# Performance work log

Hardware: AMD Instinct MI355X
Metric: run time of the kernel (lower is better)

## Reference

```python
import jax, jax.numpy as jnp
import numpy as np
from jax import lax


def _conv3x3(x, w, groups=1):
    # x: [B,C,H,W], w: [O, C//groups, 3, 3], padding=1, no bias
    return lax.conv_general_dilated(
        x, w, window_strides=(1, 1), padding=((1, 1), (1, 1)),
        dimension_numbers=('NCHW', 'OIHW', 'NCHW'),
        feature_group_count=groups)


def _nonlocal_attention(x):
    # q = k = v = flattened features; attn is [B, N, N] with N = H*W
    B, C, H, W = x.shape
    f = x.reshape(B, C, H * W)                                   # [B,C,N]
    attn = jax.nn.softmax(jnp.einsum('bcn,bcm->bnm', f, f), -1)  # [B,N,N]
    out = jnp.einsum('bnm,bcm->bcn', attn, f)                    # [B,C,N]
    return out.reshape(B, C, H, W)


def setup_inputs() -> dict:
    key = jax.random.key(0)
    k1, k2 = jax.random.split(key)
    C = 64
    x = jax.random.normal(k1, (8, C, 64, 64), dtype=jnp.float32)
    # kaiming_normal fan_out for 3x3 conv: std = sqrt(2 / (C*9))
    W_std = jax.random.normal(k2, (C, C, 3, 3), dtype=jnp.float32) * np.float32(np.sqrt(2.0 / (C * 9)))
    return {'x': x, 'W_std': W_std}


def reference(x, W_std):
    B, C, H, W = x.shape
    # FusionDiffConv: standard 3x3 conv + fixed depthwise Laplacian conv
    lap = jnp.array([[0., 1., 0.], [1., -4., 1.], [0., 1., 0.]], dtype=x.dtype)
    W_lap = jnp.broadcast_to(lap[None, None], (C, 1, 3, 3))
    feat = _conv3x3(x, W_std) + _conv3x3(x, W_lap, groups=C)
    # AttentionModule: 3-scale pooled non-local attention pyramid, bilinear upsample, sum
    out = jnp.zeros_like(feat)
    for scale in (4, 2, 1):
        h, w = H // scale, W // scale
        blk = feat.reshape(B, C, h, scale, w, scale).mean(axis=(3, 5))  # adaptive_avg_pool2d (exact divisor)
        blk = _nonlocal_attention(blk)
        # bilinear, half-pixel centers == torch align_corners=False
        out = out + jax.image.resize(blk, (B, C, H, W), method='bilinear')
    return x + out
```

## Files before the change

kernel.cpp:

```cpp
#include <hip/hip_runtime.h>
#include <hip/hip_bf16.h>
#include <math.h>

#define BB 8
#define CC 64
#define HH 64
#define WW 64
#define NPIX (HH*WW)
#define LOG2E 1.44269504088896340736f

typedef __attribute__((ext_vector_type(8))) short bf16x8;
typedef __attribute__((ext_vector_type(8))) _Float16 half8;
typedef __attribute__((ext_vector_type(4))) float floatx4;
typedef __attribute__((ext_vector_type(8))) unsigned short ushort8;

__device__ inline unsigned short f2bf(float x) {
  __hip_bfloat16 h = __float2bfloat16(x);
  return *reinterpret_cast<unsigned short*>(&h);
}
__device__ inline unsigned short f2bf_fast(float x) {
  const unsigned u = __float_as_uint(x);
  return (unsigned short)((u + 0x8000u) >> 16);
}
__device__ inline float bf2f(unsigned short u) {
  __hip_bfloat16 h = *reinterpret_cast<__hip_bfloat16*>(&u);
  return __bfloat162float(h);
}
__device__ inline unsigned short f2h(float x) {
  _Float16 h = (_Float16)x;
  return *reinterpret_cast<unsigned short*>(&h);
}
__device__ inline float h2f(unsigned short u) {
  _Float16 h = *reinterpret_cast<_Float16*>(&u);
  return (float)h;
}

__device__ inline int swzoff(int n, int c) {
  return (((c >> 3) ^ (n & 7)) << 3) | (c & 7);
}
__device__ inline int swzvslot(int key, int c) {
  return (((key >> 3) ^ (c & 7)) << 3) | (key & 7);
}

#define GLD_LDS16(gp, lp)                                                     \
  __builtin_amdgcn_global_load_lds(                                           \
      (const __attribute__((address_space(1))) void*)(gp),                    \
      (__attribute__((address_space(3))) void*)(lp), 16, 0, 0)

__global__ __launch_bounds__(256) void prep_kernel(
    const float* __restrict__ xin, const float* __restrict__ w,
    unsigned short* __restrict__ xth, unsigned short* __restrict__ xtl,
    unsigned short* __restrict__ wth, unsigned short* __restrict__ wtl) {
  __shared__ float XL[64][65];
  const int bid = blockIdx.x;
  const int tid = threadIdx.x;
  if (bid < 512) {
    const int y = bid & 63, b = bid >> 6;
    const int xq = tid & 15, cw = tid >> 4;
    const float* xb = xin + (size_t)b * CC * NPIX + y * WW;
#pragma unroll
    for (int p = 0; p < 4; ++p) {
      const int c = p * 16 + cw;
      const float4 v = *(const float4*)(xb + (size_t)c * NPIX + xq * 4);
      XL[c][xq * 4 + 0] = v.x; XL[c][xq * 4 + 1] = v.y;
      XL[c][xq * 4 + 2] = v.z; XL[c][xq * 4 + 3] = v.w;
    }
    __syncthreads();
    const int px = tid & 63, cp = tid >> 6;
    const size_t nb = ((size_t)b * NPIX + y * WW + px) * CC;
    ushort8 vh[2], vl[2];
#pragma unroll
    for (int j = 0; j < 16; ++j) {
      const float v = XL[cp * 16 + j][px];
      const unsigned short hh = f2bf(v);
      vh[j >> 3][j & 7] = hh;
      vl[j >> 3][j & 7] = f2bf(v - bf2f(hh));
    }
#pragma unroll
    for (int k = 0; k < 2; ++k) {
      const int ch = cp * 2 + k;
      const int off = ((ch ^ (px & 7)) << 3);
      *(ushort8*)(xth + nb + off) = vh[k];
      *(ushort8*)(xtl + nb + off) = vl[k];
    }
  } else {
    const int idx = (bid - 512) * 256 + tid;
    const int c   = idx & 63;
    const int o   = (idx >> 6) & 63;
    const int tap = idx >> 12;
    float v = w[((o * 64 + c) * 9) + tap];
    if (o == c) {
      const float lapk[9] = {0.f, 1.f, 0.f, 1.f, -4.f, 1.f, 0.f, 1.f, 0.f};
      v += lapk[tap];
    }
    const unsigned short hi = f2bf(v);
    wth[(tap * 64 + o) * 64 + c] = hi;
    wtl[(tap * 64 + o) * 64 + c] = f2bf(v - bf2f(hi));
  }
}

__global__ __launch_bounds__(256, 2) void conv_mfma(
    const unsigned short* __restrict__ xth,
    const unsigned short* __restrict__ xtl,
    const unsigned short* __restrict__ wth,
    const unsigned short* __restrict__ wtl,
    unsigned short* __restrict__ fh, unsigned short* __restrict__ fl,
    unsigned short* __restrict__ fv) {
  __shared__ __align__(16) unsigned short XS[6 * 4096];

  const int tid  = threadIdx.x;
  const int lane = tid & 63;
  const int wave = tid >> 6;
  const int r16  = lane & 15;
  const int quad = lane >> 4;
  const int y = blockIdx.x, b = blockIdx.y;

#pragma unroll
  for (int r = 0; r < 3; ++r) {
    const int yy = min(max(y - 1 + r, 0), HH - 1);
    const unsigned short* sh = xth + ((size_t)b * NPIX + yy * WW) * CC;
    const unsigned short* sl = xtl + ((size_t)b * NPIX + yy * WW) * CC;
    GLD_LDS16(sh + tid * 8,        &XS[r * 4096 + tid * 8]);
    GLD_LDS16(sh + 2048 + tid * 8, &XS[r * 4096 + 2048 + tid * 8]);
    GLD_LDS16(sl + tid * 8,        &XS[(3 + r) * 4096 + tid * 8]);
    GLD_LDS16(sl + 2048 + tid * 8, &XS[(3 + r) * 4096 + 2048 + tid * 8]);
  }
  __syncthreads();

  floatx4 acc[4];
#pragma unroll
  for (int t = 0; t < 4; ++t) acc[t] = (floatx4){0.f, 0.f, 0.f, 0.f};
  const bf16x8 ZF = {0, 0, 0, 0, 0, 0, 0, 0};
  const int og = wave * 16 + r16;

#pragma unroll
  for (int tap = 0; tap < 9; ++tap) {
    const int ky = tap / 3, kx = tap % 3;
    const int yy = y + ky - 1;
    if (yy < 0 || yy >= HH) continue;
    const unsigned short* wt = wth + ((tap * 64 + og) << 6);
    const unsigned short* wl = wtl + ((tap * 64 + og) << 6);
    const bf16x8 Wh0 = *(const bf16x8*)(wt + quad * 8);
    const bf16x8 Wh1 = *(const bf16x8*)(wt + 32 + quad * 8);
    const bf16x8 Wl0 = *(const bf16x8*)(wl + quad * 8);
    const bf16x8 Wl1 = *(const bf16x8*)(wl + 32 + quad * 8);
#pragma unroll
    for (int t = 0; t < 4; ++t) {
      const int px = t * 16 + r16 + kx - 1;
      const bool ok = (px >= 0) && (px < WW);
      const int pxc = ok ? px : 0;
      const int bh = ky * 4096 + pxc * 64;
      const int bl = bh + 3 * 4096;
      const int o0 = ((quad ^ (pxc & 7)) << 3);
      const int o1 = (((4 + quad) ^ (pxc & 7)) << 3);
      bf16x8 Ah0 = *(const bf16x8*)(XS + bh + o0);
      bf16x8 Ah1 = *(const bf16x8*)(XS + bh + o1);
      bf16x8 Al0 = *(const bf16x8*)(XS + bl + o0);
      bf16x8 Al1 = *(const bf16x8*)(XS + bl + o1);
      if (!ok) { Ah0 = ZF; Ah1 = ZF; Al0 = ZF; Al1 = ZF; }
      acc[t] = __builtin_amdgcn_mfma_f32_16x16x32_bf16(Ah0, Wh0, acc[t], 0, 0, 0);
      acc[t] = __builtin_amdgcn_mfma_f32_16x16x32_bf16(Ah1, Wh1, acc[t], 0, 0, 0);
      acc[t] = __builtin_amdgcn_mfma_f32_16x16x32_bf16(Ah0, Wl0, acc[t], 0, 0, 0);
      acc[t] = __builtin_amdgcn_mfma_f32_16x16x32_bf16(Ah1, Wl1, acc[t], 0, 0, 0);
      acc[t] = __builtin_amdgcn_mfma_f32_16x16x32_bf16(Al0, Wh0, acc[t], 0, 0, 0);
      acc[t] = __builtin_amdgcn_mfma_f32_16x16x32_bf16(Al1, Wh1, acc[t], 0, 0, 0);
    }
  }

#pragma unroll
  for (int t = 0; t < 4; ++t)
#pragma unroll
    for (int r = 0; r < 4; ++r) {
      const int key = t * 16 + quad * 4 + r;
      const int n = y * WW + key;
      const float v = acc[t][r];
      const unsigned short hi = f2h(v);
      const unsigned short lo = f2h(v - h2f(hi));
      fh[((size_t)b * NPIX + n) * CC + swzoff(n, og)] = hi;
      fl[((size_t)b * NPIX + n) * CC + swzoff(n, og)] = lo;
      fv[(((size_t)b * (NPIX >> 6) + y) * CC + og) * 64 + swzvslot(key, og)] =
          f2bf(v);
    }
}

__global__ void pools_kernel(const unsigned short* __restrict__ in_h,
                             const unsigned short* __restrict__ in_l,
                             unsigned short* __restrict__ h2,
                             unsigned short* __restrict__ l2,
                             unsigned short* __restrict__ v2,
                             unsigned short* __restrict__ h4,
                             unsigned short* __restrict__ l4,
                             unsigned short* __restrict__ v4) {
  const int bid = blockIdx.x;
  if (bid < 2048) {
    const int idx = bid * 256 + threadIdx.x;
    const int c  = idx & 63;
    const int t  = idx >> 6;
    const int xo = t & 31;
    const int yo = (t >> 5) & 31;
    const int b  = t >> 10;
    const size_t ibase = (size_t)b * NPIX * CC;
    float s = 0.f;
#pragma unroll
    for (int dy = 0; dy < 2; ++dy)
#pragma unroll
      for (int dx = 0; dx < 2; ++dx) {
        const int nin = (2*yo+dy) * 64 + (2*xo+dx);
        const size_t a = ibase + (size_t)nin * CC + swzoff(nin, c);
        s += h2f(in_h[a]) + h2f(in_l[a]);
      }
    const float vv = 0.25f * s;
    const unsigned short hi = f2h(vv);
    const int nout = yo * 32 + xo;
    const size_t ob = ((size_t)b * 1024 + nout) * CC + swzoff(nout, c);
    h2[ob] = hi;
    l2[ob] = f2h(vv - h2f(hi));
    v2[(((size_t)b * 16 + (nout >> 6)) * CC + c) * 64 + swzvslot(nout & 63, c)] =
        f2bf(vv);
  } else {
    const int idx = (bid - 2048) * 256 + threadIdx.x;
    const int c  = idx & 63;
    const int t  = idx >> 6;
    const int xo = t & 15;
    const int yo = (t >> 4) & 15;
    const int b  = t >> 8;
    const size_t ibase = (size_t)b * NPIX * CC;
    float s = 0.f;
#pragma unroll
    for (int dy = 0; dy < 4; ++dy)
#pragma unroll
      for (int dx = 0; dx < 4; ++dx) {
        const int nin = (4*yo+dy) * 64 + (4*xo+dx);
        const size_t a = ibase + (size_t)nin * CC + swzoff(nin, c);
        s += h2f(in_h[a]) + h2f(in_l[a]);
      }
    const float vv = 0.0625f * s;
    const unsigned short hi = f2h(vv);
    const int nout = yo * 16 + xo;
    const size_t ob = ((size_t)b * 256 + nout) * CC + swzoff(nout, c);
    h4[ob] = hi;
    l4[ob] = f2h(vv - h2f(hi));
    v4[(((size_t)b * 4 + (nout >> 6)) * CC + c) * 64 + swzvslot(nout & 63, c)] =
        f2bf(vv);
  }
}

#define STR 72

template <int NH, int KS>
__device__ __forceinline__ void attn_body(
    int bid,
    const unsigned short* __restrict__ fh,
    const unsigned short* __restrict__ fl,
    const unsigned short* __restrict__ fv,
    float* __restrict__ outF, unsigned short* __restrict__ outB,
    float* __restrict__ outL, int N,
    unsigned short* KVT, unsigned short* PtB) {
  const int tid  = threadIdx.x;
  const int lane = tid & 63;
  const int wave = tid >> 6;
  const int b    = bid & 7;
  const int rest = bid >> 3;
  const int nq   = N / (64 * NH);
  const int qt   = rest % nq;
  const int ks   = rest / nq;
  const int q0   = qt * (64 * NH) + wave * (16 * NH);
  const int nt   = (N >> 6) / KS;
  const int t0   = ks * nt;
  const int r16  = lane & 15;
  const int quad = lane >> 4;
  const int swb  = r16 & 7;

  const unsigned short* fhB = fh + (size_t)b * N * CC;
  const unsigned short* flB = fl + (size_t)b * N * CC;
  const unsigned short* fvB = fv + (size_t)b * N * CC;

  {
    const size_t tb = (size_t)t0 * 4096;
#pragma unroll
    for (int j = 0; j < 4; ++j) {
      const int cid = wave * 4 + j;
      const int arr = cid >> 3, sub = (cid & 7) << 9;
      const unsigned short* g = (arr == 0 ? fhB : fvB) + tb + sub + lane * 8;
      GLD_LDS16(g, KVT + arr * 4096 + sub + lane * 8);
    }
  }

  half8 Qh[NH][2], Ql[NH][2];
  float Mq[NH][4];
#pragma unroll
  for (int h = 0; h < NH; ++h) {
    float Mpart = 0.f;
#pragma unroll
    for (int kss = 0; kss < 2; ++kss) {
      const size_t off = (size_t)(q0 + h * 16 + r16) * CC
                         + ((((kss << 2) + quad) ^ swb) << 3);
      const ushort8 hh = *(const ushort8*)(fhB + off);
      const ushort8 ll = *(const ushort8*)(flB + off);
      half8 sh, sl;
#pragma unroll
      for (int j = 0; j < 8; ++j) {
        const float f = h2f(hh[j]) + h2f(ll[j]);
        const float g = f * LOG2E;
        const _Float16 gh = (_Float16)g;
        sh[j] = gh;
        sl[j] = (_Float16)(g - (float)gh);
        Mpart += g * f;
      }
      Qh[h][kss] = sh;
      Ql[h][kss] = sl;
    }
    Mpart += __shfl_xor(Mpart, 16, 64);
    Mpart += __shfl_xor(Mpart, 32, 64);
#pragma unroll
    for (int r = 0; r < 4; ++r) Mq[h][r] = __shfl(Mpart, quad * 4 + r, 64);
  }

  floatx4 O[NH][4];
  float lrun[NH][4];
#pragma unroll
  for (int h = 0; h < NH; ++h)
#pragma unroll
    for (int ch = 0; ch < 4; ++ch) {
      O[h][ch] = (floatx4){0.f, 0.f, 0.f, 0.f};
      lrun[h][ch] = 0.f;
    }
  unsigned short* ptw = PtB + wave * (NH * 16 * STR);

  int koff[2];
#pragma unroll
  for (int kss = 0; kss < 2; ++kss) koff[kss] = (((kss << 2) + quad) ^ swb) << 3;

  for (int t = 0; t < nt; ++t) {
    const int cur = t & 1;
    __syncthreads();
    if (t + 1 < nt) {
      const size_t tb = (size_t)(t0 + t + 1) * 4096;
      unsigned short* dst = KVT + (cur ^ 1) * 8192;
#pragma unroll
      for (int j = 0; j < 4; ++j) {
        const int cid = wave * 4 + j;
        const int arr = cid >> 3, sub = (cid & 7) << 9;
        const unsigned short* g = (arr == 0 ? fhB : fvB) + tb + sub + lane * 8;
        GLD_LDS16(g, dst + arr * 4096 + sub + lane * 8);
      }
    }
    const unsigned short* kh = KVT + cur * 8192;
    const unsigned short* vt = kh + 4096;

#pragma unroll
    for (int tt = 0; tt < 4; ++tt) {
      const int kbase = (tt * 16 + r16) * 64;
      const half8 Kh0 = *(const half8*)(kh + kbase + koff[0]);
      const half8 Kh1 = *(const half8*)(kh + kbase + koff[1]);
#pragma unroll
      for (int h = 0; h < NH; ++h) {
        floatx4 s = (floatx4){0.f, 0.f, 0.f, 0.f};
        s = __builtin_amdgcn_mfma_f32_16x16x32_f16(Qh[h][0], Kh0, s, 0, 0, 0);
        s = __builtin_amdgcn_mfma_f32_16x16x32_f16(Qh[h][1], Kh1, s, 0, 0, 0);
        s = __builtin_amdgcn_mfma_f32_16x16x32_f16(Ql[h][0], Kh0, s, 0, 0, 0);
        s = __builtin_amdgcn_mfma_f32_16x16x32_f16(Ql[h][1], Kh1, s, 0, 0, 0);
        unsigned short* pth = ptw + h * (16 * STR);
#pragma unroll
        for (int r = 0; r < 4; ++r) {
          const float p = __builtin_amdgcn_exp2f(s[r] - Mq[h][r]);
          lrun[h][r] += p;
          pth[(quad * 4 + r) * STR + tt * 16 + r16] = f2bf_fast(p);
        }
      }
    }

    bf16x8 Pf[NH][2];
#pragma unroll
    for (int h = 0; h < NH; ++h)
#pragma unroll
      for (int kss = 0; kss < 2; ++kss)
        Pf[h][kss] = *(const bf16x8*)(ptw + h * (16 * STR) + r16 * STR
                                      + kss * 32 + quad * 8);
#pragma unroll
    for (int kss = 0; kss < 2; ++kss)
#pragma unroll
      for (int ch = 0; ch < 4; ++ch) {
        const bf16x8 Vf = *(const bf16x8*)(vt + (ch * 16 + r16) * 64 + koff[kss]);
#pragma unroll
        for (int h = 0; h < NH; ++h)
          O[h][ch] = __builtin_amdgcn_mfma_f32_16x16x32_bf16(Pf[h][kss], Vf,
                                                            O[h][ch], 0, 0, 0);
      }
  }

#pragma unroll
  for (int h = 0; h < NH; ++h) {
#pragma unroll
    for (int r = 0; r < 4; ++r) {
      float lt = lrun[h][r];
      lt += __shfl_xor(lt, 1, 16);
      lt += __shfl_xor(lt, 2, 16);
      lt += __shfl_xor(lt, 4, 16);
      lt += __shfl_xor(lt, 8, 16);
      if (KS == 1) {
        lrun[h][r] = 1.f / lt;
      } else if (r16 == 0) {
        outL[(size_t)ks * BB * N + (size_t)b * N + q0 + h * 16 + quad * 4 + r] = lt;
      }
    }
#pragma unroll
    for (int ch = 0; ch < 4; ++ch)
#pragma unroll
      for (int r = 0; r < 4; ++r) {
        const size_t qi = (size_t)b * N + q0 + h * 16 + quad * 4 + r;
        if (KS == 1) {
          outF[qi * CC + ch * 16 + r16] = O[h][ch][r] * lrun[h][r];
        } else {
          outB[(size_t)ks * BB * N * CC + qi * CC + ch * 16 + r16] =
              f2bf_fast(O[h][ch][r]);
        }
      }
  }
}

__global__ __launch_bounds__(256, 3) void attn_all(
    const unsigned short* __restrict__ fh1, const unsigned short* __restrict__ fl1,
    const unsigned short* __restrict__ fv1,
    unsigned short* __restrict__ Op1, float* __restrict__ Lp1,
    const unsigned short* __restrict__ fh2, const unsigned short* __restrict__ fl2,
    const unsigned short* __restrict__ fv2,
    unsigned short* __restrict__ Op2, float* __restrict__ Lp2,
    const unsigned short* __restrict__ fh4, const unsigned short* __restrict__ fl4,
    const unsigned short* __restrict__ fv4, float* __restrict__ a4) {
  __shared__ __align__(16) unsigned short KVT[2][2 * 4096];
  __shared__ __align__(16) unsigned short Pt[4][2 * 16 * STR];
  const int bid = blockIdx.x;
  if (bid < 512) {
    attn_body<2, 2>(bid, fh1, fl1, fv1, nullptr, Op1, Lp1, NPIX,
                    &KVT[0][0], &Pt[0][0]);
  } else if (bid < 768) {
    attn_body<1, 2>(bid - 512, fh2, fl2, fv2, nullptr, Op2, Lp2, 1024,
                    &KVT[0][0], &Pt[0][0]);
  } else {
    attn_body<1, 1>(bid - 768, fh4, fl4, fv4, a4, nullptr, nullptr, 256,
                    &KVT[0][0], &Pt[0][0]);
  }
}

__global__ __launch_bounds__(256) void final3_kernel(
    const float* __restrict__ xin,
    const unsigned short* __restrict__ Op1, const float* __restrict__ Lp1,
    const unsigned short* __restrict__ Op2, const float* __restrict__ Lp2,
    const float* __restrict__ a4, float* __restrict__ out) {
  __shared__ float T[64][65];
  __shared__ float T2[64][66];
  const int tid = threadIdx.x;
  const int y = blockIdx.x & 63;
  const int b = blockIdx.x >> 6;
  const size_t S1 = (size_t)BB * NPIX * CC;
  const size_t T1 = (size_t)BB * NPIX;
  const size_t S2 = (size_t)BB * 1024 * CC;
  const size_t L2 = (size_t)BB * 1024;

  const float ty2 = y * 0.5f - 0.25f;
  const int iy2 = (int)floorf(ty2);
  const float wy2 = ty2 - iy2;
  const int iy20 = max(iy2, 0), iy21 = min(iy2 + 1, 31);

  const int nl = tid >> 2;
  const int ck = (tid & 3) * 16;

  {
    const int n = y * 64 + nl;
    float lv = Lp1[(size_t)b * NPIX + n] + Lp1[T1 + (size_t)b * NPIX + n];
    const float inv = 1.f / lv;
    float v[16];
#pragma unroll
    for (int j = 0; j < 16; ++j) v[j] = 0.f;
#pragma unroll
    for (int ks = 0; ks < 2; ++ks) {
      const unsigned short* src =
          Op1 + (size_t)ks * S1 + ((size_t)b * NPIX + n) * CC + ck;
      const ushort8 u0 = *(const ushort8*)(src);
      const ushort8 u1 = *(const ushort8*)(src + 8);
#pragma unroll
      for (int j = 0; j < 8; ++j) {
        v[j]     += bf2f(u0[j]);
        v[8 + j] += bf2f(u1[j]);
      }
    }
#pragma unroll
    for (int j = 0; j < 16; ++j) T[ck + j][nl] = v[j] * inv;
  }
  {
    const int row = nl >> 5;
    const int ix  = nl & 31;
    const int n2  = (row == 0 ? iy20 : iy21) * 32 + ix;
    float lv = Lp2[(size_t)b * 1024 + n2] + Lp2[L2 + (size_t)b * 1024 + n2];
    const float inv = 1.f / lv;
    float v[16];
#pragma unroll
    for (int j = 0; j < 16; ++j) v[j] = 0.f;
#pragma unroll
    for (int ks = 0; ks < 2; ++ks) {
      const unsigned short* src =
          Op2 + (size_t)ks * S2 + ((size_t)b * 1024 + n2) * CC + ck;
      const ushort8 u0 = *(const ushort8*)(src);
      const ushort8 u1 = *(const ushort8*)(src + 8);
#pragma unroll
      for (int j = 0; j < 8; ++j) {
        v[j]     += bf2f(u0[j]);
        v[8 + j] += bf2f(u1[j]);
      }
    }
#pragma unroll
    for (int j = 0; j < 16; ++j) T2[ck + j][nl] = v[j] * inv;
  }
  __syncthreads();

  const int c  = tid >> 2;
  const int xk = (tid & 3) * 16;
  const float* xrow = xin + (((size_t)b * CC + c) * HH + y) * WW;
  float* orow = out + (((size_t)b * CC + c) * HH + y) * WW;

  const float ty4 = y * 0.25f - 0.375f;
  const int iy4 = (int)floorf(ty4);
  const float wy4 = ty4 - iy4;
  const int iy40 = max(iy4, 0), iy41 = min(iy4 + 1, 15);
  const float* b4 = a4 + (size_t)b * 256 * 64 + c;

#pragma unroll
  for (int j = 0; j < 16; ++j) {
    const int xx = xk + j;
    float r = xrow[xx] + T[c][xx];
    {
      const float tx = xx * 0.5f - 0.25f;
      const int ix = (int)floorf(tx);
      const float wx = tx - ix;
      const int ix0 = max(ix, 0), ix1 = min(ix + 1, 31);
      const float v00 = T2[c][ix0],      v01 = T2[c][ix1];
      const float v10 = T2[c][32 + ix0], v11 = T2[c][32 + ix1];
      r += (1.f-wy2)*((1.f-wx)*v00 + wx*v01) + wy2*((1.f-wx)*v10 + wx*v11);
    }
    {
      const float tx = xx * 0.25f - 0.375f;
      const int ix = (int)floorf(tx);
      const float wx = tx - ix;
      const int ix0 = max(ix, 0), ix1 = min(ix + 1, 15);
      const float v00 = b4[(iy40*16+ix0)*64], v01 = b4[(iy40*16+ix1)*64];
      const float v10 = b4[(iy41*16+ix0)*64], v11 = b4[(iy41*16+ix1)*64];
      r += (1.f-wy4)*((1.f-wx)*v00 + wx*v01) + wy4*((1.f-wx)*v10 + wx*v11);
    }
    orow[xx] = r;
  }
}

extern "C" void kernel_launch(void* const* d_in, const int* in_sizes, int n_in,
                              void* d_out, int out_size, void* d_ws,
                              size_t ws_size, hipStream_t stream) {
  const float* x = (const float*)d_in[0];
  const float* w = (const float*)d_in[1];
  float* out = (float*)d_out;

  unsigned short* fh1 = (unsigned short*)d_ws;
  unsigned short* fl1 = fh1 + (size_t)BB*NPIX*CC;
  unsigned short* fv1 = fl1 + (size_t)BB*NPIX*CC;
  unsigned short* fh2 = fv1 + (size_t)BB*NPIX*CC;
  unsigned short* fl2 = fh2 + (size_t)BB*1024*CC;
  unsigned short* fv2 = fl2 + (size_t)BB*1024*CC;
  unsigned short* fh4 = fv2 + (size_t)BB*1024*CC;
  unsigned short* fl4 = fh4 + (size_t)BB*256*CC;
  unsigned short* fv4 = fl4 + (size_t)BB*256*CC;
  unsigned short* Op1 = fv4 + (size_t)BB*256*CC;
  float* Lp1 = (float*)(Op1 + 2*(size_t)BB*NPIX*CC);
  unsigned short* Op2 = (unsigned short*)(Lp1 + 2*(size_t)BB*NPIX);
  float* Lp2 = (float*)(Op2 + 2*(size_t)BB*1024*CC);
  float* a4  = Lp2 + 2*(size_t)BB*1024;

  unsigned short* xth = (unsigned short*)Op1;
  unsigned short* xtl = xth + (size_t)BB*NPIX*CC;
  unsigned short* wth = (unsigned short*)Op2;
  unsigned short* wtl = wth + 9*64*64;

  prep_kernel<<<656, 256, 0, stream>>>(x, w, xth, xtl, wth, wtl);
  conv_mfma<<<dim3(64, 8), 256, 0, stream>>>(xth, xtl, wth, wtl, fh1, fl1, fv1);
  pools_kernel<<<2560, 256, 0, stream>>>(fh1, fl1, fh2, fl2, fv2, fh4, fl4, fv4);
  attn_all<<<800, 256, 0, stream>>>(fh1, fl1, fv1, Op1, Lp1,
                                    fh2, fl2, fv2, Op2, Lp2,
                                    fh4, fl4, fv4, a4);
  final3_kernel<<<512, 256, 0, stream>>>(x, Op1, Lp1, Op2, Lp2, a4, out);
}
```

Measured before the change: 165.7 us.

## Compute transposed scores and feed P directly from registers into PV MFMA

Swaps the QK^T MFMA operands so each lane holds score values laid out as the A-operand of a 16x16x16 f16 MFMA. The exponentiated probabilities are then packed into half4 and multiplied with V straight from registers, which removes the LDS round trip for P (the Pt buffer and its stores and loads). V is switched from bf16 to fp16 to match, and the row-sum reduction is restructured. Freeing the LDS and registers lets the launch bound target 4 blocks per CU, at the cost of more, smaller MFMAs and fp16 range limits for V.

After: 156.1 us. 5.8% less time.

```diff
diff --git a/kernel.cpp b/kernel.cpp
--- a/kernel.cpp
+++ b/kernel.cpp
@@ -11,6 +11,7 @@
 
 typedef __attribute__((ext_vector_type(8))) short bf16x8;
 typedef __attribute__((ext_vector_type(8))) _Float16 half8;
+typedef __attribute__((ext_vector_type(4))) _Float16 half4;
 typedef __attribute__((ext_vector_type(4))) float floatx4;
 typedef __attribute__((ext_vector_type(8))) unsigned short ushort8;
 
@@ -179,7 +180,7 @@
       fh[((size_t)b * NPIX + n) * CC + swzoff(n, og)] = hi;
       fl[((size_t)b * NPIX + n) * CC + swzoff(n, og)] = lo;
       fv[(((size_t)b * (NPIX >> 6) + y) * CC + og) * 64 + swzvslot(key, og)] =
-          f2bf(v);
+          f2h(v);
     }
 }
 
@@ -216,7 +217,7 @@
     h2[ob] = hi;
     l2[ob] = f2h(vv - h2f(hi));
     v2[(((size_t)b * 16 + (nout >> 6)) * CC + c) * 64 + swzvslot(nout & 63, c)] =
-        f2bf(vv);
+        f2h(vv);
   } else {
     const int idx = (bid - 2048) * 256 + threadIdx.x;
     const int c  = idx & 63;
@@ -241,11 +242,9 @@
     h4[ob] = hi;
     l4[ob] = f2h(vv - h2f(hi));
     v4[(((size_t)b * 4 + (nout >> 6)) * CC + c) * 64 + swzvslot(nout & 63, c)] =
-        f2bf(vv);
-  }
-}
-
-#define STR 72
+        f2h(vv);
+  }
+}
 
 template <int NH, int KS>
 __device__ __forceinline__ void attn_body(
@@ -255,7 +254,7 @@
     const unsigned short* __restrict__ fv,
     float* __restrict__ outF, unsigned short* __restrict__ outB,
     float* __restrict__ outL, int N,
-    unsigned short* KVT, unsigned short* PtB) {
+    unsigned short* KVT) {
   const int tid  = threadIdx.x;
   const int lane = tid & 63;
   const int wave = tid >> 6;
@@ -287,7 +286,7 @@
   }
 
   half8 Qh[NH][2], Ql[NH][2];
-  float Mq[NH][4];
+  float Mq[NH];
 #pragma unroll
   for (int h = 0; h < NH; ++h) {
     float Mpart = 0.f;
@@ -312,24 +311,22 @@
     }
     Mpart += __shfl_xor(Mpart, 16, 64);
     Mpart += __shfl_xor(Mpart, 32, 64);
-#pragma unroll
-    for (int r = 0; r < 4; ++r) Mq[h][r] = __shfl(Mpart, quad * 4 + r, 64);
+    Mq[h] = Mpart;
   }
 
   floatx4 O[NH][4];
-  float lrun[NH][4];
-#pragma unroll
-  for (int h = 0; h < NH; ++h)
-#pragma unroll
-    for (int ch = 0; ch < 4; ++ch) {
-      O[h][ch] = (floatx4){0.f, 0.f, 0.f, 0.f};
-      lrun[h][ch] = 0.f;
-    }
-  unsigned short* ptw = PtB + wave * (NH * 16 * STR);
+  float lloc[NH];
+#pragma unroll
+  for (int h = 0; h < NH; ++h) {
+    lloc[h] = 0.f;
+#pragma unroll
+    for (int ch = 0; ch < 4; ++ch) O[h][ch] = (floatx4){0.f, 0.f, 0.f, 0.f};
+  }
 
   int koff[2];
 #pragma unroll
   for (int kss = 0; kss < 2; ++kss) koff[kss] = (((kss << 2) + quad) ^ swb) << 3;
+  const int vq = ((quad & 1) << 2);
 
   for (int t = 0; t < nt; ++t) {
     const int cur = t & 1;
@@ -353,56 +350,45 @@
       const int kbase = (tt * 16 + r16) * 64;
       const half8 Kh0 = *(const half8*)(kh + kbase + koff[0]);
       const half8 Kh1 = *(const half8*)(kh + kbase + koff[1]);
+      const int vslot = (((tt * 2 + (quad >> 1)) ^ swb) << 3) + vq;
+      half4 Vf[4];
+#pragma unroll
+      for (int ch = 0; ch < 4; ++ch)
+        Vf[ch] = *(const half4*)(vt + (ch * 16 + r16) * 64 + vslot);
 #pragma unroll
       for (int h = 0; h < NH; ++h) {
         floatx4 s = (floatx4){0.f, 0.f, 0.f, 0.f};
-        s = __builtin_amdgcn_mfma_f32_16x16x32_f16(Qh[h][0], Kh0, s, 0, 0, 0);
-        s = __builtin_amdgcn_mfma_f32_16x16x32_f16(Qh[h][1], Kh1, s, 0, 0, 0);
-        s = __builtin_amdgcn_mfma_f32_16x16x32_f16(Ql[h][0], Kh0, s, 0, 0, 0);
-        s = __builtin_amdgcn_mfma_f32_16x16x32_f16(Ql[h][1], Kh1, s, 0, 0, 0);
-        unsigned short* pth = ptw + h * (16 * STR);
-#pragma unroll
-        for (int r = 0; r < 4; ++r) {
-          const float p = __builtin_amdgcn_exp2f(s[r] - Mq[h][r]);
-          lrun[h][r] += p;
-          pth[(quad * 4 + r) * STR + tt * 16 + r16] = f2bf_fast(p);
-        }
-      }
-    }
-
-    bf16x8 Pf[NH][2];
-#pragma unroll
-    for (int h = 0; h < NH; ++h)
-#pragma unroll
-      for (int kss = 0; kss < 2; ++kss)
-        Pf[h][kss] = *(const bf16x8*)(ptw + h * (16 * STR) + r16 * STR
-                                      + kss * 32 + quad * 8);
-#pragma unroll
-    for (int kss = 0; kss < 2; ++kss)
-#pragma unroll
-      for (int ch = 0; ch < 4; ++ch) {
-        const bf16x8 Vf = *(const bf16x8*)(vt + (ch * 16 + r16) * 64 + koff[kss]);
-#pragma unroll
-        for (int h = 0; h < NH; ++h)
-          O[h][ch] = __builtin_amdgcn_mfma_f32_16x16x32_bf16(Pf[h][kss], Vf,
-                                                            O[h][ch], 0, 0, 0);
-      }
+        s = __builtin_amdgcn_mfma_f32_16x16x32_f16(Kh0, Qh[h][0], s, 0, 0, 0);
+        s = __builtin_amdgcn_mfma_f32_16x16x32_f16(Kh1, Qh[h][1], s, 0, 0, 0);
+        s = __builtin_amdgcn_mfma_f32_16x16x32_f16(Kh0, Ql[h][0], s, 0, 0, 0);
+        s = __builtin_amdgcn_mfma_f32_16x16x32_f16(Kh1, Ql[h][1], s, 0, 0, 0);
+        const float p0 = __builtin_amdgcn_exp2f(s[0] - Mq[h]);
+        const float p1 = __builtin_amdgcn_exp2f(s[1] - Mq[h]);
+        const float p2 = __builtin_amdgcn_exp2f(s[2] - Mq[h]);
+        const float p3 = __builtin_amdgcn_exp2f(s[3] - Mq[h]);
+        lloc[h] += (p0 + p1) + (p2 + p3);
+        const half4 Pf = {(_Float16)p0, (_Float16)p1, (_Float16)p2, (_Float16)p3};
+#pragma unroll
+        for (int ch = 0; ch < 4; ++ch)
+          O[h][ch] = __builtin_amdgcn_mfma_f32_16x16x16f16(Pf, Vf[ch],
+                                                           O[h][ch], 0, 0, 0);
+      }
+    }
   }
 
 #pragma unroll
   for (int h = 0; h < NH; ++h) {
-#pragma unroll
-    for (int r = 0; r < 4; ++r) {
-      float lt = lrun[h][r];
-      lt += __shfl_xor(lt, 1, 16);
-      lt += __shfl_xor(lt, 2, 16);
-      lt += __shfl_xor(lt, 4, 16);
-      lt += __shfl_xor(lt, 8, 16);
-      if (KS == 1) {
-        lrun[h][r] = 1.f / lt;
-      } else if (r16 == 0) {
-        outL[(size_t)ks * BB * N + (size_t)b * N + q0 + h * 16 + quad * 4 + r] = lt;
-      }
+    float lt = lloc[h];
+    lt += __shfl_xor(lt, 16, 64);
+    lt += __shfl_xor(lt, 32, 64);
+    float lq[4];
+#pragma unroll
+    for (int r = 0; r < 4; ++r) lq[r] = __shfl(lt, quad * 4 + r, 16);
+    if (KS != 1 && r16 == 0) {
+#pragma unroll
+      for (int r = 0; r < 4; ++r)
+        outL[(size_t)ks * BB * N + (size_t)b * N + q0 + h * 16 + quad * 4 + r] =
+            lq[r];
     }
 #pragma unroll
     for (int ch = 0; ch < 4; ++ch)
@@ -410,7 +396,7 @@
       for (int r = 0; r < 4; ++r) {
         const size_t qi = (size_t)b * N + q0 + h * 16 + quad * 4 + r;
         if (KS == 1) {
-          outF[qi * CC + ch * 16 + r16] = O[h][ch][r] * lrun[h][r];
+          outF[qi * CC + ch * 16 + r16] = O[h][ch][r] / lq[r];
         } else {
           outB[(size_t)ks * BB * N * CC + qi * CC + ch * 16 + r16] =
               f2bf_fast(O[h][ch][r]);
@@ -419,7 +405,7 @@
   }
 }
 
-__global__ __launch_bounds__(256, 3) void attn_all(
+__global__ __launch_bounds__(256, 4) void attn_all(
     const unsigned short* __restrict__ fh1, const unsigned short* __restrict__ fl1,
     const unsigned short* __restrict__ fv1,
     unsigned short* __restrict__ Op1, float* __restrict__ Lp1,
@@ -429,17 +415,15 @@
     const unsigned short* __restrict__ fh4, const unsigned short* __restrict__ fl4,
     const unsigned short* __restrict__ fv4, float* __restrict__ a4) {
   __shared__ __align__(16) unsigned short KVT[2][2 * 4096];
-  __shared__ __align__(16) unsigned short Pt[4][2 * 16 * STR];
   const int bid = blockIdx.x;
   if (bid < 512) {
-    attn_body<2, 2>(bid, fh1, fl1, fv1, nullptr, Op1, Lp1, NPIX,
-                    &KVT[0][0], &Pt[0][0]);
+    attn_body<2, 2>(bid, fh1, fl1, fv1, nullptr, Op1, Lp1, NPIX, &KVT[0][0]);
   } else if (bid < 768) {
     attn_body<1, 2>(bid - 512, fh2, fl2, fv2, nullptr, Op2, Lp2, 1024,
-                    &KVT[0][0], &Pt[0][0]);
+                    &KVT[0][0]);
   } else {
     attn_body<1, 1>(bid - 768, fh4, fl4, fv4, a4, nullptr, nullptr, 256,
-                    &KVT[0][0], &Pt[0][0]);
+                    &KVT[0][0]);
   }
 }
 
```
